# Kernel tuning notes

Measured on AMD Instinct MI355X. Metric: run time of the kernel, lower is better.

The kernel has to match this reference:

```python
import jax, jax.numpy as jnp
import numpy as np

B, T, S0 = 8, 4, 4096
D_MODEL, H, D, R, RANK = 2048, 16, 128, 64, 512
C = D - R  # content dim = 64


def _rope(x, positions):
    # x: [B, H, T, R]; rotate-half style RoPE as in the torch module
    half = x.shape[-1] // 2
    inv_freq = 1.0 / (10000.0 ** (jnp.arange(half, dtype=jnp.float32) / half))
    freqs = positions.astype(jnp.float32)[:, None] * inv_freq[None, :]  # [T, half]
    cos = jnp.cos(freqs)[None, None].astype(x.dtype)
    sin = jnp.sin(freqs)[None, None].astype(x.dtype)
    x1, x2 = x[..., :half], x[..., half:]
    return jnp.concatenate([x1 * cos - x2 * sin, x1 * sin + x2 * cos], axis=-1)


def setup_inputs() -> dict:
    key = jax.random.key(0)
    ks = jax.random.split(key, 9)
    s = 0.02
    return {
        "x": jax.random.normal(ks[0], (B, T, D_MODEL), jnp.float32),
        "cache_c_kv": jax.random.normal(ks[1], (B, S0, RANK), jnp.float32),
        "cache_k_rope": jax.random.normal(ks[2], (B, S0, H, R), jnp.float32),
        "w_q": jax.random.normal(ks[3], (D_MODEL, H * C), jnp.float32) * s,
        "w_q_rope": jax.random.normal(ks[4], (D_MODEL, H * R), jnp.float32) * s,
        "w_kv_down": jax.random.normal(ks[5], (D_MODEL, RANK), jnp.float32) * s,
        "w_kv_up": jax.random.normal(ks[6], (RANK, H * D), jnp.float32) * s,
        "w_k_rope": jax.random.normal(ks[7], (D_MODEL, H * R), jnp.float32) * s,
        "w_out": jax.random.normal(ks[8], (H * D, D_MODEL), jnp.float32) * s,
    }


def reference(x, cache_c_kv, cache_k_rope, w_q, w_q_rope, w_kv_down, w_kv_up, w_k_rope, w_out):
    cache_len = cache_c_kv.shape[1]
    positions = jnp.arange(cache_len, cache_len + T)

    # queries
    q_content = (x @ w_q).reshape(B, T, H, C).transpose(0, 2, 1, 3)        # [B,H,T,C]
    q_rope = (x @ w_q_rope).reshape(B, T, H, R).transpose(0, 2, 1, 3)      # [B,H,T,R]
    q_rope = _rope(q_rope, positions)
    q = jnp.concatenate([q_content, q_rope], axis=-1)                       # [B,H,T,D]

    # new compressed kv + rope keys, append to cache
    c_kv_new = x @ w_kv_down                                                # [B,T,RANK]
    k_rope_new = (x @ w_k_rope).reshape(B, T, H, R).transpose(0, 2, 1, 3)
    k_rope_new = _rope(k_rope_new, positions).transpose(0, 2, 1, 3)         # [B,T,H,R]
    c_kv = jnp.concatenate([cache_c_kv, c_kv_new], axis=1)                  # [B,S,RANK]
    k_rope = jnp.concatenate([cache_k_rope, k_rope_new], axis=1)            # [B,S,H,R]

    # decompress full cache every step (the expensive MLA pattern)
    S = c_kv.shape[1]
    kv = (c_kv @ w_kv_up).reshape(B, S, H, D)                               # [B,S,H,D]
    k_content = kv[..., :C].transpose(0, 2, 1, 3)                           # [B,H,S,C]
    v = kv.transpose(0, 2, 1, 3)                                            # [B,H,S,D]
    k = jnp.concatenate([k_content, k_rope.transpose(0, 2, 1, 3)], axis=-1) # [B,H,S,D]

    # kv_cache present => is_prefill False => no causal mask (faithful to source)
    scale = 1.0 / jnp.sqrt(jnp.asarray(D, dtype=q.dtype))
    scores = jnp.einsum('bhtd,bhsd->bhts', q, k) * scale
    attn = jax.nn.softmax(scores, axis=-1)
    out = jnp.einsum('bhts,bhsd->bhtd', attn, v)                            # [B,H,T,D]
    out = out.transpose(0, 2, 1, 3).reshape(B, T, H * D)
    return out @ w_out                                                       # [B,T,D_MODEL]
```

## Files before the change

### kernel.cpp

```cpp
#include <hip/hip_runtime.h>
#include <hip/hip_fp16.h>
#include <cmath>

#define BB 8
#define TT 4
#define HH 16
#define DDIM 128
#define RRDIM 64
#define CCDIM 64
#define RANKC 512
#define DMODEL 2048
#define S0C 4096
#define NQ 64
#define HD 2048
#define NACT 3584
#define NSC 65
#define NG 17
#define SPAD 4160
#define SCALE_ATT 0.08838834764831845f

typedef __attribute__((ext_vector_type(8))) short bf16x8;
typedef __attribute__((ext_vector_type(4))) float f32x4;
typedef unsigned short ushortT;

#define AIDX(row, kk) ((row)*132 + (((row)>>2)<<2) + (kk))

static __device__ __forceinline__ unsigned short f2bf(float x) {
  unsigned u = __float_as_uint(x);
  u += 0x7FFFu + ((u >> 16) & 1u);
  return (unsigned short)(u >> 16);
}
static __device__ __forceinline__ unsigned pk2(float a, float b) {
  return (unsigned)f2bf(a) | ((unsigned)f2bf(b) << 16);
}

__global__ __launch_bounds__(256) void k_front(const float* __restrict__ A,
                                               const float* __restrict__ w0,
                                               const float* __restrict__ w1,
                                               const float* __restrict__ w2,
                                               const float* __restrict__ w3,
                                               const float* __restrict__ cckv,
                                               float* __restrict__ part,
                                               ushortT* __restrict__ ckvB,
                                               ushortT* __restrict__ ckvT,
                                               float* __restrict__ rctab) {
  __shared__ float shf[4352];
  const int tid = threadIdx.x;
  const int bx = blockIdx.x;
  if (bx < 448) {
    const int cb = bx % 28;
    const int k0 = (bx / 28) * 128;
    const float* W; int N, lc0, off;
    if (cb < 8)       { W = w0; N = 1024; lc0 = cb * 128;        off = 0; }
    else if (cb < 16) { W = w1; N = 1024; lc0 = (cb - 8) * 128;  off = 1024; }
    else if (cb < 20) { W = w2; N = 512;  lc0 = (cb - 16) * 128; off = 2048; }
    else              { W = w3; N = 1024; lc0 = (cb - 20) * 128; off = 2560; }
    {
      const int row = tid >> 3;
      const int kseg = (tid & 7) * 16;
      const float4* s4 = reinterpret_cast<const float4*>(A + (size_t)row * DMODEL + k0 + kseg);
      float4 v0 = s4[0], v1 = s4[1], v2 = s4[2], v3 = s4[3];
      *reinterpret_cast<float4*>(&shf[AIDX(row, kseg)])      = v0;
      *reinterpret_cast<float4*>(&shf[AIDX(row, kseg + 4)])  = v1;
      *reinterpret_cast<float4*>(&shf[AIDX(row, kseg + 8)])  = v2;
      *reinterpret_cast<float4*>(&shf[AIDX(row, kseg + 12)]) = v3;
    }
    __syncthreads();
    const int cg = tid & 31;
    const int rg = tid >> 5;
    float acc[4][4];
    #pragma unroll
    for (int r = 0; r < 4; ++r)
      #pragma unroll
      for (int c = 0; c < 4; ++c) acc[r][c] = 0.f;
    #pragma unroll 4
    for (int kk = 0; kk < 128; ++kk) {
      const float4 w4 = *reinterpret_cast<const float4*>(W + (size_t)(k0 + kk) * N + lc0 + cg * 4);
      const float wv[4] = {w4.x, w4.y, w4.z, w4.w};
      #pragma unroll
      for (int r = 0; r < 4; ++r) {
        const float av = shf[AIDX(rg * 4 + r, kk)];
        #pragma unroll
        for (int c = 0; c < 4; ++c) acc[r][c] = fmaf(av, wv[c], acc[r][c]);
      }
    }
    #pragma unroll
    for (int r = 0; r < 4; ++r) {
      float4 o = make_float4(acc[r][0], acc[r][1], acc[r][2], acc[r][3]);
      *reinterpret_cast<float4*>(part + ((size_t)(bx / 28) * 32 + rg * 4 + r) * NACT + off + lc0 + cg * 4) = o;
    }
  } else if (bx < 960) {
    ushortT* tlds = reinterpret_cast<ushortT*>(shf);
    const int idx = bx - 448;
    const int b = idx >> 6, c = idx & 63;
    const float* src = cckv + ((size_t)b * S0C + c * 64) * RANKC;
    ushortT* dstB = ckvB + ((size_t)(b * NSC + c) * 64) * RANKC;
    ushortT* dstT = ckvT + ((size_t)(b * NSC + c) * RANKC) * 64;
    const int s = tid >> 2, rq = tid & 3;
    const int rloc = tid >> 1, shalf = (tid & 1) * 32;
    for (int slab = 0; slab < 4; ++slab) {
      const int r0 = slab * 128;
      unsigned pk_arr[16];
      #pragma unroll
      for (int i = 0; i < 8; ++i) {
        const float4 v = *reinterpret_cast<const float4*>(src + (size_t)s * RANKC + r0 + rq * 32 + i * 4);
        pk_arr[2 * i]     = pk2(v.x, v.y);
        pk_arr[2 * i + 1] = pk2(v.z, v.w);
        *reinterpret_cast<uint2*>(&tlds[s * 136 + rq * 32 + i * 4]) =
            make_uint2(pk_arr[2 * i], pk_arr[2 * i + 1]);
      }
      {
        uint4* db = reinterpret_cast<uint4*>(dstB + (size_t)s * RANKC + r0 + rq * 32);
        db[0] = make_uint4(pk_arr[0], pk_arr[1], pk_arr[2], pk_arr[3]);
        db[1] = make_uint4(pk_arr[4], pk_arr[5], pk_arr[6], pk_arr[7]);
        db[2] = make_uint4(pk_arr[8], pk_arr[9], pk_arr[10], pk_arr[11]);
        db[3] = make_uint4(pk_arr[12], pk_arr[13], pk_arr[14], pk_arr[15]);
      }
      __syncthreads();
      unsigned pkv[16];
      #pragma unroll
      for (int k = 0; k < 16; ++k) {
        const unsigned t0 = tlds[(shalf + 2 * k)     * 136 + rloc];
        const unsigned t1 = tlds[(shalf + 2 * k + 1) * 136 + rloc];
        pkv[k] = t0 | (t1 << 16);
      }
      uint4* d = reinterpret_cast<uint4*>(dstT + ((size_t)(r0 + rloc)) * 64 + shalf);
      d[0] = make_uint4(pkv[0], pkv[1], pkv[2], pkv[3]);
      d[1] = make_uint4(pkv[4], pkv[5], pkv[6], pkv[7]);
      d[2] = make_uint4(pkv[8], pkv[9], pkv[10], pkv[11]);
      d[3] = make_uint4(pkv[12], pkv[13], pkv[14], pkv[15]);
      __syncthreads();
    }
  } else {
    const int b = bx - 960;
    const uint4 z = make_uint4(0, 0, 0, 0);
    uint4* p = reinterpret_cast<uint4*>(ckvT + ((size_t)(b * NSC + 64) * RANKC) * 64);
    for (int i = tid; i < 4096; i += 256) p[i] = z;
    uint4* q = reinterpret_cast<uint4*>(ckvB + (((size_t)(b * NSC + 64) * 64) + 4) * RANKC);
    for (int i = tid; i < 3840; i += 256) q[i] = z;
    if (bx == 960 && tid < 128) {
      const int t = tid >> 5, j = tid & 31;
      const double fr = (double)(S0C + t) * pow(10000.0, -(double)j / 32.0);
      rctab[t * 32 + j]       = (float)cos(fr);
      rctab[128 + t * 32 + j] = (float)sin(fr);
    }
  }
}

__global__ __launch_bounds__(256) void k_mid(const float* __restrict__ part0,
                                             const float* __restrict__ cache_kr,
                                             const float* __restrict__ wup,
                                             const float* __restrict__ rctab,
                                             ushortT* __restrict__ qlat,
                                             ushortT* __restrict__ ckvB,
                                             ushortT* __restrict__ ckvT,
                                             __half* __restrict__ rs) {
  __shared__ float smid[10880];
  const int tid = threadIdx.x;
  const int bx = blockIdx.x;
  if (bx < 1152) {
    const int bh = bx / 9, sy = bx % 9;
    const int b = bh >> 4, h = bh & 15;
    float* raw_q = smid;
    float* raw_k = smid + 256;
    float* qr_l  = smid + 512;
    float* kr_l  = smid + 768;
    {
      const int t = tid >> 6, j = tid & 63;
      const size_t rowoff = (size_t)(b * TT + t) * NACT;
      float sq = 0.f, sk = 0.f;
      #pragma unroll 4
      for (int ks = 0; ks < 16; ++ks) {
        const float* pp = part0 + (size_t)ks * (32 * NACT) + rowoff;
        sq += pp[1024 + h * 64 + j];
        sk += pp[2560 + h * 64 + j];
      }
      raw_q[t * 64 + j] = sq;
      raw_k[t * 64 + j] = sk;
    }
    __syncthreads();
    {
      const int t = tid >> 6, j = tid & 63;
      const int j2 = j & 31;
      const float cs = rctab[t * 32 + j2];
      const float sn = rctab[128 + t * 32 + j2];
      const float qa = raw_q[t * 64 + j], qp = raw_q[t * 64 + (j ^ 32)];
      const float ka = raw_k[t * 64 + j], kp = raw_k[t * 64 + (j ^ 32)];
      float qv, kv;
      if (j < 32) { qv = qa * cs - qp * sn; kv = ka * cs - kp * sn; }
      else        { qv = qp * sn + qa * cs; kv = kp * sn + ka * cs; }
      qr_l[t * 64 + j] = qv * SCALE_ATT;
      kr_l[t * 64 + j] = kv;
    }
    __syncthreads();
    const int ql = tid & 3;
    float4 qf[4][4];
    #pragma unroll
    for (int t = 0; t < 4; ++t)
      #pragma unroll
      for (int u = 0; u < 4; ++u)
        qf[t][u] = *reinterpret_cast<const float4*>(&qr_l[t * 64 + ql * 16 + u * 4]);
    const int s0 = sy * 512;
    #pragma unroll 1
    for (int pass = 0; pass < 8; ++pass) {
      const int s = s0 + pass * 64 + (tid >> 2);
      if (s < 4100) {
        float p[4] = {0.f, 0.f, 0.f, 0.f};
        const float* krow = (s < S0C)
            ? cache_kr + (((size_t)b * S0C + s) * HH + h) * RRDIM
            : &kr_l[(s - S0C) * 64];
        #pragma unroll
        for (int u = 0; u < 4; ++u) {
          const float4 kv = *reinterpret_cast<const float4*>(krow + ql * 16 + u * 4);
          #pragma unroll
          for (int t = 0; t < 4; ++t)
            p[t] += kv.x * qf[t][u].x + kv.y * qf[t][u].y
                  + kv.z * qf[t][u].z + kv.w * qf[t][u].w;
        }
        #pragma unroll
        for (int t = 0; t < 4; ++t) {
          p[t] += __shfl_xor(p[t], 1, 4);
          p[t] += __shfl_xor(p[t], 2, 4);
        }
        rs[((size_t)bh * 4 + ql) * SPAD + s] = __float2half(p[ql]);
      }
    }
  } else if (bx < 1216) {
    const int lx = bx - 1152;
    const int h = lx & 15;
    const int r0 = (lx >> 4) * 128;
    float* wt  = smid;
    float* a_s = smid + 8448;
    {
      const int r = tid >> 1;
      const int cseg = (tid & 1) * 32;
      const float* src = wup + (size_t)(r0 + r) * HD + h * DDIM + cseg;
      #pragma unroll
      for (int u = 0; u < 8; ++u) {
        const float4 v = *reinterpret_cast<const float4*>(src + u * 4);
        wt[(cseg + u * 4 + 0) * 132 + r] = v.x;
        wt[(cseg + u * 4 + 1) * 132 + r] = v.y;
        wt[(cseg + u * 4 + 2) * 132 + r] = v.z;
        wt[(cseg + u * 4 + 3) * 132 + r] = v.w;
      }
    }
    {
      const int bt = tid >> 3;
      const int c8 = (tid & 7) * 8;
      float v[8] = {0.f,0.f,0.f,0.f,0.f,0.f,0.f,0.f};
      #pragma unroll 4
      for (int ks = 0; ks < 16; ++ks) {
        const float4* pp = reinterpret_cast<const float4*>(
            part0 + (size_t)ks * (32 * NACT) + (size_t)bt * NACT + h * CCDIM + c8);
        const float4 x0 = pp[0], x1 = pp[1];
        v[0]+=x0.x; v[1]+=x0.y; v[2]+=x0.z; v[3]+=x0.w;
        v[4]+=x1.x; v[5]+=x1.y; v[6]+=x1.z; v[7]+=x1.w;
      }
      #pragma unroll
      for (int u = 0; u < 8; ++u) a_s[bt * 68 + c8 + u] = v[u];
    }
    __syncthreads();
    const int r = tid & 127;
    const int bth = tid >> 7;
    float acc[16];
    #pragma unroll
    for (int i = 0; i < 16; ++i) acc[i] = 0.f;
    #pragma unroll 8
    for (int c = 0; c < 64; ++c) {
      const float wv = wt[c * 132 + r];
      #pragma unroll
      for (int i = 0; i < 16; ++i)
        acc[i] = fmaf(a_s[(bth * 16 + i) * 68 + c], wv, acc[i]);
    }
    #pragma unroll
    for (int i = 0; i < 16; ++i) {
      const int bt = bth * 16 + i;
      const int b = bt >> 2, t = bt & 3;
      qlat[((size_t)(b * NQ) + h * TT + t) * RANKC + r0 + r] = f2bf(acc[i]);
    }
  } else {
    const int g = (bx - 1216) * 256 + tid;
    const int r = g & 511;
    const int bt = g >> 9;
    const int b = bt >> 2, t = bt & 3;
    float s = 0.f;
    #pragma unroll 4
    for (int ks = 0; ks < 16; ++ks)
      s += part0[(size_t)ks * (32 * NACT) + (size_t)bt * NACT + 2048 + r];
    const ushortT bv = f2bf(s);
    ckvB[(((size_t)(b * NSC + 64) * 64) + t) * RANKC + r] = bv;
    ckvT[(((size_t)(b * NSC + 64) * RANKC) + r) * 64 + t] = bv;
  }
}

__global__ __launch_bounds__(256) void k_score(
    const ushortT* __restrict__ ckvB, const ushortT* __restrict__ qlat,
    const __half* __restrict__ rs, float* __restrict__ ml,
    ushortT* __restrict__ Pg) {
  __shared__ ushortT PL[64 * 72];
  const int tid = threadIdx.x;
  const int wv = tid >> 6;
  const int lane = tid & 63;
  const int lm = lane & 15, lg = lane >> 4;
  const int b = blockIdx.x, chunk = blockIdx.y;
  const int qbase = wv * 16;
  const int scnt = (chunk < 64) ? 64 : TT;
  const ushortT* bsrc = ckvB + ((size_t)(b * NSC + chunk) * 64) * RANKC;

  const ushortT* qrow = qlat + ((size_t)b * NQ + qbase + lm) * RANKC + lg * 8;
  bf16x8 qa[16];
  #pragma unroll
  for (int ks = 0; ks < 16; ++ks)
    qa[ks] = *reinterpret_cast<const bf16x8*>(qrow + ks * 32);

  f32x4 acc[4];
  #pragma unroll
  for (int st = 0; st < 4; ++st) acc[st] = (f32x4){0.f, 0.f, 0.f, 0.f};
  #pragma unroll
  for (int ks = 0; ks < 16; ++ks) {
    #pragma unroll
    for (int st = 0; st < 4; ++st) {
      const bf16x8 bf = *reinterpret_cast<const bf16x8*>(
          bsrc + (size_t)(st * 16 + lm) * RANKC + ks * 32 + lg * 8);
      acc[st] = __builtin_amdgcn_mfma_f32_16x16x32_bf16(qa[ks], bf, acc[st], 0, 0, 0);
    }
  }

  #pragma unroll
  for (int reg = 0; reg < 4; ++reg) {
    const int qi = qbase + lg * 4 + reg;
    const __half* rp = rs + (((size_t)(b * HH) + (qi >> 2)) * TT + (qi & 3)) * SPAD + chunk * 64;
    float vvv[4];
    float mx = -1e30f;
    #pragma unroll
    for (int st = 0; st < 4; ++st) {
      const int sl = st * 16 + lm;
      const float val = (sl < scnt)
          ? fmaf(acc[st][reg], SCALE_ATT, __half2float(rp[sl]))
          : -1e30f;
      vvv[st] = val;
      mx = fmaxf(mx, val);
    }
    #pragma unroll
    for (int off = 1; off < 16; off <<= 1) mx = fmaxf(mx, __shfl_xor(mx, off, 16));
    float sum = 0.f;
    #pragma unroll
    for (int st = 0; st < 4; ++st) {
      const float p = __expf(vvv[st] - mx);
      vvv[st] = p;
      sum += p;
    }
    #pragma unroll
    for (int off = 1; off < 16; off <<= 1) sum += __shfl_xor(sum, off, 16);
    #pragma unroll
    for (int st = 0; st < 4; ++st)
      PL[(qbase + lg * 4 + reg) * 72 + st * 16 + lm] = f2bf(vvv[st]);
    if (lm == 0) {
      const size_t mb = (((size_t)b * NSC + chunk) * NQ + qi) * 2;
      ml[mb] = mx; ml[mb + 1] = sum;
    }
  }
  __syncthreads();
  {
    const int row = tid >> 2, seg = (tid & 3) * 16;
    const uint4* sp = reinterpret_cast<const uint4*>(&PL[row * 72 + seg]);
    uint4* dp = reinterpret_cast<uint4*>(
        Pg + ((size_t)(b * NSC + chunk) * NQ + row) * 64 + seg);
    dp[0] = sp[0]; dp[1] = sp[1];
  }
}

__global__ __launch_bounds__(256) void k_pv(
    const ushortT* __restrict__ ckvT, const ushortT* __restrict__ Pg,
    const float* __restrict__ ml, float* __restrict__ olat,
    float* __restrict__ mlg) {
  const int tid = threadIdx.x;
  const int wv = tid >> 6;
  const int lane = tid & 63;
  const int lm = lane & 15, lg = lane >> 4;
  const int b = blockIdx.x, g = blockIdx.y, rg = blockIdx.z;
  const int qbase = wv * 16;
  const int nc = (g < 16) ? 4 : 1;
  const int c0 = (g < 16) ? g * 4 : 64;

  float m_cl = -1e30f, l_cl = 0.f;
  if (lg < nc) {
    const size_t mb = (((size_t)b * NSC + c0 + lg) * NQ + qbase + lm) * 2;
    m_cl = ml[mb]; l_cl = ml[mb + 1];
  }
  float mg = fmaxf(m_cl, __shfl_xor(m_cl, 16));
  mg = fmaxf(mg, __shfl_xor(mg, 32));
  const float wgt = (lg < nc) ? __expf(m_cl - mg) : 0.f;
  float la = l_cl * wgt;
  la += __shfl_xor(la, 16);
  la += __shfl_xor(la, 32);
  if (rg == 0 && lg == 0) {
    const size_t gb = (((size_t)b * NG + g) * NQ + qbase + lm) * 2;
    mlg[gb] = mg; mlg[gb + 1] = la;
  }
  float wf[4][4];
  #pragma unroll
  for (int c = 0; c < 4; ++c)
    #pragma unroll
    for (int reg = 0; reg < 4; ++reg)
      wf[c][reg] = __shfl(wgt, c * 16 + lg * 4 + reg);

  f32x4 OACC[8];
  #pragma unroll
  for (int nt = 0; nt < 8; ++nt) OACC[nt] = (f32x4){0.f, 0.f, 0.f, 0.f};

  for (int c = 0; c < nc; ++c) {
    const ushortT* pb = Pg + ((size_t)(b * NSC + c0 + c) * NQ + qbase + lm) * 64 + lg * 8;
    const bf16x8 pa0 = *reinterpret_cast<const bf16x8*>(pb);
    const bf16x8 pa1 = *reinterpret_cast<const bf16x8*>(pb + 32);
    const ushortT* vb = ckvT + (((size_t)(b * NSC + c0 + c) * RANKC) + rg * 128 + lm) * 64 + lg * 8;
    f32x4 a2[8];
    #pragma unroll
    for (int nt = 0; nt < 8; ++nt) a2[nt] = (f32x4){0.f, 0.f, 0.f, 0.f};
    #pragma unroll
    for (int nt = 0; nt < 8; ++nt) {
      const bf16x8 b0 = *reinterpret_cast<const bf16x8*>(vb + (size_t)nt * 16 * 64);
      const bf16x8 b1 = *reinterpret_cast<const bf16x8*>(vb + (size_t)nt * 16 * 64 + 32);
      a2[nt] = __builtin_amdgcn_mfma_f32_16x16x32_bf16(pa0, b0, a2[nt], 0, 0, 0);
      a2[nt] = __builtin_amdgcn_mfma_f32_16x16x32_bf16(pa1, b1, a2[nt], 0, 0, 0);
    }
    const f32x4 wv4 = {wf[c][0], wf[c][1], wf[c][2], wf[c][3]};
    #pragma unroll
    for (int nt = 0; nt < 8; ++nt) OACC[nt] += wv4 * a2[nt];
  }

  const size_t obase = ((size_t)(b * NG + g) * NQ) * RANKC;
  #pragma unroll
  for (int nt = 0; nt < 8; ++nt)
    #pragma unroll
    for (int reg = 0; reg < 4; ++reg)
      olat[obase + (size_t)(qbase + lg * 4 + reg) * RANKC + rg * 128 + nt * 16 + lm] = OACC[nt][reg];
}

__global__ __launch_bounds__(512) void k_combF(const float* __restrict__ mlg,
                                               const float* __restrict__ olat,
                                               const float* __restrict__ wup,
                                               float* __restrict__ ohead) {
  __shared__ float wrow[4][20];
  __shared__ float att_lds[4][516];
  const int h = blockIdx.x, b = blockIdx.y;
  const int tid = threadIdx.x;
  const int wave = tid >> 6;
  const int i = wave >> 1;
  const int rhalf = wave & 1;
  const int rl = tid & 63;
  const int qi = h * TT + i;
  float m1 = -1e30f, l1 = 0.f;
  if (rl < NG) {
    const size_t base = (((size_t)b * NG + rl) * NQ + qi) * 2;
    m1 = mlg[base]; l1 = mlg[base + 1];
  }
  float M = m1;
  #pragma unroll
  for (int off = 1; off < 64; off <<= 1) M = fmaxf(M, __shfl_xor(M, off));
  float L = (rl < NG) ? l1 * __expf(m1 - M) : 0.f;
  #pragma unroll
  for (int off = 1; off < 64; off <<= 1) L += __shfl_xor(L, off);
  const float invL = 1.0f / L;
  if (rl < NG) wrow[i][rl] = __expf(m1 - M) * invL;
  __syncthreads();
  const int r0 = rhalf * 256 + rl * 4;
  float o0 = 0.f, o1 = 0.f, o2 = 0.f, o3 = 0.f;
  for (int c = 0; c < NG; ++c) {
    const float w = wrow[i][c];
    const float4 v = *reinterpret_cast<const float4*>(
        olat + (((size_t)b * NG + c) * NQ + qi) * RANKC + r0);
    o0 = fmaf(v.x, w, o0); o1 = fmaf(v.y, w, o1);
    o2 = fmaf(v.z, w, o2); o3 = fmaf(v.w, w, o3);
  }
  *reinterpret_cast<float4*>(&att_lds[i][r0]) = make_float4(o0, o1, o2, o3);
  __syncthreads();
  const int col = tid & 127;
  const int t = tid >> 7;
  float acc = 0.f;
  #pragma unroll 8
  for (int r = 0; r < RANKC; ++r)
    acc = fmaf(att_lds[t][r], wup[(size_t)r * HD + h * DDIM + col], acc);
  ohead[(size_t)(b * TT + t) * HD + h * DDIM + col] = acc;
}

__global__ __launch_bounds__(256) void k_proj(const float* __restrict__ A,
                                              const float* __restrict__ W,
                                              float* __restrict__ part,
                                              int N, int NTOT, int coloff) {
  __shared__ float a_lds[4352];
  const int tid = threadIdx.x;
  const int c0 = blockIdx.x * 128;
  const int k0 = blockIdx.y * 128;
  {
    const int row = tid >> 3;
    const int kseg = (tid & 7) * 16;
    const float4* s4 = reinterpret_cast<const float4*>(A + (size_t)row * DMODEL + k0 + kseg);
    float4 v0 = s4[0], v1 = s4[1], v2 = s4[2], v3 = s4[3];
    *reinterpret_cast<float4*>(&a_lds[AIDX(row, kseg)])      = v0;
    *reinterpret_cast<float4*>(&a_lds[AIDX(row, kseg + 4)])  = v1;
    *reinterpret_cast<float4*>(&a_lds[AIDX(row, kseg + 8)])  = v2;
    *reinterpret_cast<float4*>(&a_lds[AIDX(row, kseg + 12)]) = v3;
  }
  __syncthreads();
  const int cg = tid & 31;
  const int rg = tid >> 5;
  float acc[4][4];
  #pragma unroll
  for (int r = 0; r < 4; ++r)
    #pragma unroll
    for (int c = 0; c < 4; ++c) acc[r][c] = 0.f;
  #pragma unroll 4
  for (int kk = 0; kk < 128; ++kk) {
    const float4 w4 = *reinterpret_cast<const float4*>(W + (size_t)(k0 + kk) * N + c0 + cg * 4);
    const float wv[4] = {w4.x, w4.y, w4.z, w4.w};
    #pragma unroll
    for (int r = 0; r < 4; ++r) {
      const float av = a_lds[AIDX(rg * 4 + r, kk)];
      #pragma unroll
      for (int c = 0; c < 4; ++c) acc[r][c] = fmaf(av, wv[c], acc[r][c]);
    }
  }
  #pragma unroll
  for (int r = 0; r < 4; ++r) {
    float4 o = make_float4(acc[r][0], acc[r][1], acc[r][2], acc[r][3]);
    *reinterpret_cast<float4*>(part + ((size_t)blockIdx.y * 32 + rg * 4 + r) * NTOT + coloff + c0 + cg * 4) = o;
  }
}

__global__ __launch_bounds__(256) void k_reduce(const float* __restrict__ part,
                                                float* __restrict__ out, int total, int nsplit) {
  int g = blockIdx.x * 256 + threadIdx.x;
  if (g >= total) return;
  float s = 0.f;
  #pragma unroll 4
  for (int c = 0; c < nsplit; ++c) s += part[(size_t)c * total + g];
  out[g] = s;
}

extern "C" void kernel_launch(void* const* d_in, const int* in_sizes, int n_in,
                              void* d_out, int out_size, void* d_ws, size_t ws_size,
                              hipStream_t stream) {
  const float* x     = (const float*)d_in[0];
  const float* cckv  = (const float*)d_in[1];
  const float* ckr   = (const float*)d_in[2];
  const float* w_q   = (const float*)d_in[3];
  const float* w_qr  = (const float*)d_in[4];
  const float* w_kvd = (const float*)d_in[5];
  const float* w_kvu = (const float*)d_in[6];
  const float* w_kr  = (const float*)d_in[7];
  const float* w_out = (const float*)d_in[8];
  float* out = (float*)d_out;
  float* ws = (float*)d_ws;

  size_t off = 0;
  ushortT* qlat   = (ushortT*)(ws + off); off += 131072;
  float* mlb      = ws + off; off += (size_t)BB * NSC * NQ * 2;
  float* mlgb     = ws + off; off += (size_t)BB * NG * NQ * 2;
  float* ohead    = ws + off; off += 65536;
  float* rctab    = ws + off; off += 256;
  __half* rsb     = (__half*)(ws + off); off += 1064960;
  ushortT* ckvB   = (ushortT*)(ws + off); off += 8519680;
  ushortT* ckvT   = (ushortT*)(ws + off); off += 8519680;
  ushortT* Pgb    = (ushortT*)(ws + off); off += 1064960;
  float* regB  = ws + off;
  float* part0 = regB;
  float* olat  = regB;
  float* part3 = regB;

  k_front<<<dim3(968), 256, 0, stream>>>(x, w_q, w_qr, w_kvd, w_kr, cckv, part0, ckvB, ckvT, rctab);
  k_mid<<<dim3(1280), 256, 0, stream>>>(part0, ckr, w_kvu, rctab, qlat, ckvB, ckvT, rsb);
  k_score<<<dim3(BB, NSC), 256, 0, stream>>>(ckvB, qlat, rsb, mlb, Pgb);
  k_pv<<<dim3(BB, NG, 4), 256, 0, stream>>>(ckvT, Pgb, mlb, olat, mlgb);
  k_combF<<<dim3(16, 8), 512, 0, stream>>>(mlgb, olat, w_kvu, ohead);
  k_proj<<<dim3(16, 16), 256, 0, stream>>>(ohead, w_out, part3, 2048, 2048, 0);
  k_reduce<<<dim3(256), 256, 0, stream>>>(part3, out, 32 * HD, 16);
}
```

Before: 213.2 us.

## Move cache conversion into mid kernel, atomic-reduce output projection, split combine reduction

```diff
diff --git a/kernel.cpp b/kernel.cpp
--- a/kernel.cpp
+++ b/kernel.cpp
@@ -39,7 +39,6 @@
                                                const float* __restrict__ w1,
                                                const float* __restrict__ w2,
                                                const float* __restrict__ w3,
-                                               const float* __restrict__ cckv,
                                                float* __restrict__ part,
                                                ushortT* __restrict__ ckvB,
                                                ushortT* __restrict__ ckvT,
@@ -89,56 +88,14 @@
       float4 o = make_float4(acc[r][0], acc[r][1], acc[r][2], acc[r][3]);
       *reinterpret_cast<float4*>(part + ((size_t)(bx / 28) * 32 + rg * 4 + r) * NACT + off + lc0 + cg * 4) = o;
     }
-  } else if (bx < 960) {
-    ushortT* tlds = reinterpret_cast<ushortT*>(shf);
-    const int idx = bx - 448;
-    const int b = idx >> 6, c = idx & 63;
-    const float* src = cckv + ((size_t)b * S0C + c * 64) * RANKC;
-    ushortT* dstB = ckvB + ((size_t)(b * NSC + c) * 64) * RANKC;
-    ushortT* dstT = ckvT + ((size_t)(b * NSC + c) * RANKC) * 64;
-    const int s = tid >> 2, rq = tid & 3;
-    const int rloc = tid >> 1, shalf = (tid & 1) * 32;
-    for (int slab = 0; slab < 4; ++slab) {
-      const int r0 = slab * 128;
-      unsigned pk_arr[16];
-      #pragma unroll
-      for (int i = 0; i < 8; ++i) {
-        const float4 v = *reinterpret_cast<const float4*>(src + (size_t)s * RANKC + r0 + rq * 32 + i * 4);
-        pk_arr[2 * i]     = pk2(v.x, v.y);
-        pk_arr[2 * i + 1] = pk2(v.z, v.w);
-        *reinterpret_cast<uint2*>(&tlds[s * 136 + rq * 32 + i * 4]) =
-            make_uint2(pk_arr[2 * i], pk_arr[2 * i + 1]);
-      }
-      {
-        uint4* db = reinterpret_cast<uint4*>(dstB + (size_t)s * RANKC + r0 + rq * 32);
-        db[0] = make_uint4(pk_arr[0], pk_arr[1], pk_arr[2], pk_arr[3]);
-        db[1] = make_uint4(pk_arr[4], pk_arr[5], pk_arr[6], pk_arr[7]);
-        db[2] = make_uint4(pk_arr[8], pk_arr[9], pk_arr[10], pk_arr[11]);
-        db[3] = make_uint4(pk_arr[12], pk_arr[13], pk_arr[14], pk_arr[15]);
-      }
-      __syncthreads();
-      unsigned pkv[16];
-      #pragma unroll
-      for (int k = 0; k < 16; ++k) {
-        const unsigned t0 = tlds[(shalf + 2 * k)     * 136 + rloc];
-        const unsigned t1 = tlds[(shalf + 2 * k + 1) * 136 + rloc];
-        pkv[k] = t0 | (t1 << 16);
-      }
-      uint4* d = reinterpret_cast<uint4*>(dstT + ((size_t)(r0 + rloc)) * 64 + shalf);
-      d[0] = make_uint4(pkv[0], pkv[1], pkv[2], pkv[3]);
-      d[1] = make_uint4(pkv[4], pkv[5], pkv[6], pkv[7]);
-      d[2] = make_uint4(pkv[8], pkv[9], pkv[10], pkv[11]);
-      d[3] = make_uint4(pkv[12], pkv[13], pkv[14], pkv[15]);
-      __syncthreads();
-    }
   } else {
-    const int b = bx - 960;
+    const int b = bx - 448;
     const uint4 z = make_uint4(0, 0, 0, 0);
     uint4* p = reinterpret_cast<uint4*>(ckvT + ((size_t)(b * NSC + 64) * RANKC) * 64);
     for (int i = tid; i < 4096; i += 256) p[i] = z;
     uint4* q = reinterpret_cast<uint4*>(ckvB + (((size_t)(b * NSC + 64) * 64) + 4) * RANKC);
     for (int i = tid; i < 3840; i += 256) q[i] = z;
-    if (bx == 960 && tid < 128) {
+    if (bx == 448 && tid < 128) {
       const int t = tid >> 5, j = tid & 31;
       const double fr = (double)(S0C + t) * pow(10000.0, -(double)j / 32.0);
       rctab[t * 32 + j]       = (float)cos(fr);
@@ -151,6 +108,7 @@
                                              const float* __restrict__ cache_kr,
                                              const float* __restrict__ wup,
                                              const float* __restrict__ rctab,
+                                             const float* __restrict__ cckv,
                                              ushortT* __restrict__ qlat,
                                              ushortT* __restrict__ ckvB,
                                              ushortT* __restrict__ ckvT,
@@ -201,7 +159,7 @@
       for (int u = 0; u < 4; ++u)
         qf[t][u] = *reinterpret_cast<const float4*>(&qr_l[t * 64 + ql * 16 + u * 4]);
     const int s0 = sy * 512;
-    #pragma unroll 1
+    #pragma unroll 2
     for (int pass = 0; pass < 8; ++pass) {
       const int s = s0 + pass * 64 + (tid >> 2);
       if (s < 4100) {
@@ -278,7 +236,7 @@
       const int b = bt >> 2, t = bt & 3;
       qlat[((size_t)(b * NQ) + h * TT + t) * RANKC + r0 + r] = f2bf(acc[i]);
     }
-  } else {
+  } else if (bx < 1280) {
     const int g = (bx - 1216) * 256 + tid;
     const int r = g & 511;
     const int bt = g >> 9;
@@ -290,6 +248,48 @@
     const ushortT bv = f2bf(s);
     ckvB[(((size_t)(b * NSC + 64) * 64) + t) * RANKC + r] = bv;
     ckvT[(((size_t)(b * NSC + 64) * RANKC) + r) * 64 + t] = bv;
+  } else {
+    ushortT* tlds = reinterpret_cast<ushortT*>(smid);
+    const int idx = bx - 1280;
+    const int b = idx >> 6, c = idx & 63;
+    const float* src = cckv + ((size_t)b * S0C + c * 64) * RANKC;
+    ushortT* dstB = ckvB + ((size_t)(b * NSC + c) * 64) * RANKC;
+    ushortT* dstT = ckvT + ((size_t)(b * NSC + c) * RANKC) * 64;
+    const int s = tid >> 2, rq = tid & 3;
+    const int rloc = tid >> 1, shalf = (tid & 1) * 32;
+    for (int slab = 0; slab < 4; ++slab) {
+      const int r0 = slab * 128;
+      unsigned pk_arr[16];
+      #pragma unroll
+      for (int i = 0; i < 8; ++i) {
+        const float4 v = *reinterpret_cast<const float4*>(src + (size_t)s * RANKC + r0 + rq * 32 + i * 4);
+        pk_arr[2 * i]     = pk2(v.x, v.y);
+        pk_arr[2 * i + 1] = pk2(v.z, v.w);
+        *reinterpret_cast<uint2*>(&tlds[s * 136 + rq * 32 + i * 4]) =
+            make_uint2(pk_arr[2 * i], pk_arr[2 * i + 1]);
+      }
+      {
+        uint4* db = reinterpret_cast<uint4*>(dstB + (size_t)s * RANKC + r0 + rq * 32);
+        db[0] = make_uint4(pk_arr[0], pk_arr[1], pk_arr[2], pk_arr[3]);
+        db[1] = make_uint4(pk_arr[4], pk_arr[5], pk_arr[6], pk_arr[7]);
+        db[2] = make_uint4(pk_arr[8], pk_arr[9], pk_arr[10], pk_arr[11]);
+        db[3] = make_uint4(pk_arr[12], pk_arr[13], pk_arr[14], pk_arr[15]);
+      }
+      __syncthreads();
+      unsigned pkv[16];
+      #pragma unroll
+      for (int k = 0; k < 16; ++k) {
+        const unsigned t0 = tlds[(shalf + 2 * k)     * 136 + rloc];
+        const unsigned t1 = tlds[(shalf + 2 * k + 1) * 136 + rloc];
+        pkv[k] = t0 | (t1 << 16);
+      }
+      uint4* d = reinterpret_cast<uint4*>(dstT + ((size_t)(r0 + rloc)) * 64 + shalf);
+      d[0] = make_uint4(pkv[0], pkv[1], pkv[2], pkv[3]);
+      d[1] = make_uint4(pkv[4], pkv[5], pkv[6], pkv[7]);
+      d[2] = make_uint4(pkv[8], pkv[9], pkv[10], pkv[11]);
+      d[3] = make_uint4(pkv[12], pkv[13], pkv[14], pkv[15]);
+      __syncthreads();
+    }
   }
 }
 
@@ -440,11 +440,17 @@
 __global__ __launch_bounds__(512) void k_combF(const float* __restrict__ mlg,
                                                const float* __restrict__ olat,
                                                const float* __restrict__ wup,
-                                               float* __restrict__ ohead) {
+                                               float* __restrict__ ohead,
+                                               float* __restrict__ out) {
   __shared__ float wrow[4][20];
   __shared__ float att_lds[4][516];
+  __shared__ float red[4][4][32][4];
   const int h = blockIdx.x, b = blockIdx.y;
   const int tid = threadIdx.x;
+  {
+    const int t = tid >> 7, col = tid & 127;
+    out[(size_t)(b * TT + t) * HD + h * DDIM + col] = 0.f;
+  }
   const int wave = tid >> 6;
   const int i = wave >> 1;
   const int rhalf = wave & 1;
@@ -465,29 +471,49 @@
   if (rl < NG) wrow[i][rl] = __expf(m1 - M) * invL;
   __syncthreads();
   const int r0 = rhalf * 256 + rl * 4;
-  float o0 = 0.f, o1 = 0.f, o2 = 0.f, o3 = 0.f;
-  for (int c = 0; c < NG; ++c) {
-    const float w = wrow[i][c];
-    const float4 v = *reinterpret_cast<const float4*>(
-        olat + (((size_t)b * NG + c) * NQ + qi) * RANKC + r0);
-    o0 = fmaf(v.x, w, o0); o1 = fmaf(v.y, w, o1);
-    o2 = fmaf(v.z, w, o2); o3 = fmaf(v.w, w, o3);
-  }
-  *reinterpret_cast<float4*>(&att_lds[i][r0]) = make_float4(o0, o1, o2, o3);
+  {
+    float o0 = 0.f, o1 = 0.f, o2 = 0.f, o3 = 0.f;
+    for (int c = 0; c < NG; ++c) {
+      const float w = wrow[i][c];
+      const float4 v = *reinterpret_cast<const float4*>(
+          olat + (((size_t)b * NG + c) * NQ + qi) * RANKC + r0);
+      o0 = fmaf(v.x, w, o0); o1 = fmaf(v.y, w, o1);
+      o2 = fmaf(v.z, w, o2); o3 = fmaf(v.w, w, o3);
+    }
+    *reinterpret_cast<float4*>(&att_lds[i][r0]) = make_float4(o0, o1, o2, o3);
+  }
   __syncthreads();
-  const int col = tid & 127;
   const int t = tid >> 7;
-  float acc = 0.f;
-  #pragma unroll 8
-  for (int r = 0; r < RANKC; ++r)
-    acc = fmaf(att_lds[t][r], wup[(size_t)r * HD + h * DDIM + col], acc);
-  ohead[(size_t)(b * TT + t) * HD + h * DDIM + col] = acc;
-}
-
-__global__ __launch_bounds__(256) void k_proj(const float* __restrict__ A,
-                                              const float* __restrict__ W,
-                                              float* __restrict__ part,
-                                              int N, int NTOT, int coloff) {
+  const int rq = (tid >> 5) & 3;
+  const int c4 = tid & 31;
+  const float* wb = wup + (size_t)h * DDIM + c4 * 4;
+  float a0 = 0.f, a1 = 0.f, a2 = 0.f, a3 = 0.f;
+  const int rbeg = rq * 128;
+  #pragma unroll 4
+  for (int rr = 0; rr < 128; ++rr) {
+    const int r = rbeg + rr;
+    const float4 w4 = *reinterpret_cast<const float4*>(wb + (size_t)r * HD);
+    const float a = att_lds[t][r];
+    a0 = fmaf(a, w4.x, a0); a1 = fmaf(a, w4.y, a1);
+    a2 = fmaf(a, w4.z, a2); a3 = fmaf(a, w4.w, a3);
+  }
+  *reinterpret_cast<float4*>(&red[rq][t][c4][0]) = make_float4(a0, a1, a2, a3);
+  __syncthreads();
+  if (tid < 128) {
+    const int t2 = tid >> 5, c42 = tid & 31;
+    float4 s = make_float4(0.f, 0.f, 0.f, 0.f);
+    #pragma unroll
+    for (int q = 0; q < 4; ++q) {
+      const float4 v = *reinterpret_cast<const float4*>(&red[q][t2][c42][0]);
+      s.x += v.x; s.y += v.y; s.z += v.z; s.w += v.w;
+    }
+    *reinterpret_cast<float4*>(&ohead[(size_t)(b * TT + t2) * HD + h * DDIM + c42 * 4]) = s;
+  }
+}
+
+__global__ __launch_bounds__(256) void k_projA(const float* __restrict__ A,
+                                               const float* __restrict__ W,
+                                               float* __restrict__ out) {
   __shared__ float a_lds[4352];
   const int tid = threadIdx.x;
   const int c0 = blockIdx.x * 128;
@@ -512,7 +538,7 @@
     for (int c = 0; c < 4; ++c) acc[r][c] = 0.f;
   #pragma unroll 4
   for (int kk = 0; kk < 128; ++kk) {
-    const float4 w4 = *reinterpret_cast<const float4*>(W + (size_t)(k0 + kk) * N + c0 + cg * 4);
+    const float4 w4 = *reinterpret_cast<const float4*>(W + (size_t)(k0 + kk) * HD + c0 + cg * 4);
     const float wv[4] = {w4.x, w4.y, w4.z, w4.w};
     #pragma unroll
     for (int r = 0; r < 4; ++r) {
@@ -522,20 +548,10 @@
     }
   }
   #pragma unroll
-  for (int r = 0; r < 4; ++r) {
-    float4 o = make_float4(acc[r][0], acc[r][1], acc[r][2], acc[r][3]);
-    *reinterpret_cast<float4*>(part + ((size_t)blockIdx.y * 32 + rg * 4 + r) * NTOT + coloff + c0 + cg * 4) = o;
-  }
-}
-
-__global__ __launch_bounds__(256) void k_reduce(const float* __restrict__ part,
-                                                float* __restrict__ out, int total, int nsplit) {
-  int g = blockIdx.x * 256 + threadIdx.x;
-  if (g >= total) return;
-  float s = 0.f;
-  #pragma unroll 4
-  for (int c = 0; c < nsplit; ++c) s += part[(size_t)c * total + g];
-  out[g] = s;
+  for (int r = 0; r < 4; ++r)
+    #pragma unroll
+    for (int c = 0; c < 4; ++c)
+      unsafeAtomicAdd(&out[(size_t)(rg * 4 + r) * HD + c0 + cg * 4 + c], acc[r][c]);
 }
 
 extern "C" void kernel_launch(void* const* d_in, const int* in_sizes, int n_in,
@@ -566,13 +582,11 @@
   float* regB  = ws + off;
   float* part0 = regB;
   float* olat  = regB;
-  float* part3 = regB;
-
-  k_front<<<dim3(968), 256, 0, stream>>>(x, w_q, w_qr, w_kvd, w_kr, cckv, part0, ckvB, ckvT, rctab);
-  k_mid<<<dim3(1280), 256, 0, stream>>>(part0, ckr, w_kvu, rctab, qlat, ckvB, ckvT, rsb);
+
+  k_front<<<dim3(456), 256, 0, stream>>>(x, w_q, w_qr, w_kvd, w_kr, part0, ckvB, ckvT, rctab);
+  k_mid<<<dim3(1792), 256, 0, stream>>>(part0, ckr, w_kvu, rctab, cckv, qlat, ckvB, ckvT, rsb);
   k_score<<<dim3(BB, NSC), 256, 0, stream>>>(ckvB, qlat, rsb, mlb, Pgb);
   k_pv<<<dim3(BB, NG, 4), 256, 0, stream>>>(ckvT, Pgb, mlb, olat, mlgb);
-  k_combF<<<dim3(16, 8), 512, 0, stream>>>(mlgb, olat, w_kvu, ohead);
-  k_proj<<<dim3(16, 16), 256, 0, stream>>>(ohead, w_out, part3, 2048, 2048, 0);
-  k_reduce<<<dim3(256), 256, 0, stream>>>(part3, out, 32 * HD, 16);
-}
+  k_combF<<<dim3(16, 8), 512, 0, stream>>>(mlgb, olat, w_kvu, ohead, out);
+  k_projA<<<dim3(16, 16), 256, 0, stream>>>(ohead, w_out, out);
+}
```

Result: slower. 219.2 us (+2.8%).
